# Kernel tuning notes

Hardware: AMD Instinct MI355X
Metric: run time of the kernel (lower is better)

Reference implementation:

```python
import jax, jax.numpy as jnp
import numpy as np

N_BINS = 15  # init kwarg n_bins


def setup_inputs() -> dict:
    key = jax.random.key(0)
    k1, k2, k3, k4 = jax.random.split(key, 4)
    B, T = 8192, 4096
    confidences = jax.random.uniform(k1, (B, T), dtype=jnp.float32)
    predictions = jax.random.randint(k2, (B, T), 0, 3, dtype=jnp.int32)
    targets = jax.random.randint(k3, (B, T), 0, 3, dtype=jnp.int32)
    mask = jax.random.randint(k4, (B, T), 0, 2, dtype=jnp.int32)
    return {"confidences": confidences, "predictions": predictions,
            "targets": targets, "mask": mask}


def reference(confidences, predictions, targets, mask):
    # Flatten, as in the torch forward.
    c = confidences.reshape(-1)
    p = predictions.reshape(-1)
    t = targets.reshape(-1)
    w = mask.reshape(-1).astype(c.dtype)  # 1.0 where valid, 0.0 where masked out

    n = N_BINS
    # Bin b covers (b/n, (b+1)/n]: for c in (0,1], bin index = ceil(c*n) - 1.
    idx = jnp.clip(jnp.ceil(c * n).astype(jnp.int32) - 1, 0, n - 1)
    # c == 0 falls in no bin (strict lower bound on first bin), c > 1 in none.
    in_range = ((c > 0.0) & (c <= 1.0)).astype(c.dtype)
    wv = w * in_range  # effective per-element weight for bin statistics

    counts = jax.ops.segment_sum(wv, idx, num_segments=n)              # n_b
    conf_sum = jax.ops.segment_sum(wv * c, idx, num_segments=n)        # sum conf per bin
    corr = (p == t).astype(c.dtype)
    corr_sum = jax.ops.segment_sum(wv * corr, idx, num_segments=n)     # sum correct per bin

    total = jnp.sum(w)  # len(confidences) after masking
    safe = jnp.maximum(counts, jnp.asarray(1.0, c.dtype))
    avg_conf = conf_sum / safe
    acc = corr_sum / safe
    ece = jnp.sum(jnp.where(counts > 0, jnp.abs(avg_conf - acc) * counts / total, 0.0))
    return ece
```

## Files before the change

kernel.cpp:

```cpp
#include <hip/hip_runtime.h>

#define NBINS 15

typedef float f32x4 __attribute__((ext_vector_type(4)));
typedef int   i32x4 __attribute__((ext_vector_type(4)));


__global__ __launch_bounds__(256, 8) void ece_partial(
    const float* __restrict__ conf,
    const int*   __restrict__ pred,
    const int*   __restrict__ targ,
    const int*   __restrict__ mask,
    unsigned long long* __restrict__ ws,
    int nvec)
{
    __shared__ unsigned int h[4][16];
    __shared__ unsigned long long stot;

    const int tid = threadIdx.x;
    const int wid = tid >> 6;

    if (tid < 64) h[tid >> 4][tid & 15] = 0u;
    if (tid == 0) stot = 0ULL;
    __syncthreads();

    const int gid    = blockIdx.x * blockDim.x + tid;
    const int stride = gridDim.x * blockDim.x;

    const f32x4* __restrict__ c4p = (const f32x4*)conf;
    const i32x4* __restrict__ p4p = (const i32x4*)pred;
    const i32x4* __restrict__ t4p = (const i32x4*)targ;
    const i32x4* __restrict__ m4p = (const i32x4*)mask;

    unsigned int tot = 0;

    int i = gid;
    for (; i + stride < nvec; i += 2 * stride) {
        const int j = i + stride;
        f32x4 c0 = c4p[i];
        f32x4 c1 = c4p[j];
        i32x4 p0 = p4p[i];
        i32x4 p1 = p4p[j];
        i32x4 t0 = t4p[i];
        i32x4 t1 = t4p[j];
        i32x4 m0 = m4p[i];
        i32x4 m1 = m4p[j];
        asm volatile("" : "+v"(c0), "+v"(c1), "+v"(p0), "+v"(p1),
                          "+v"(t0), "+v"(t1), "+v"(m0), "+v"(m1));

#pragma unroll
        for (int k = 0; k < 4; ++k) {
            float c = c0[k];
            int   m = m0[k];
            tot += (unsigned int)m;
            if ((m != 0) & (c > 0.0f) & (c <= 1.0f)) {
                int bin = (int)ceilf(c * 15.0f) - 1;
                bin = min(max(bin, 0), NBINS - 1);
                float corr = (p0[k] == t0[k]) ? 1.0f : 0.0f;
                int d = (int)rintf((c - corr) * 65536.0f);
                atomicAdd(&h[wid][bin], (unsigned int)d);
            }
        }
#pragma unroll
        for (int k = 0; k < 4; ++k) {
            float c = c1[k];
            int   m = m1[k];
            tot += (unsigned int)m;
            if ((m != 0) & (c > 0.0f) & (c <= 1.0f)) {
                int bin = (int)ceilf(c * 15.0f) - 1;
                bin = min(max(bin, 0), NBINS - 1);
                float corr = (p1[k] == t1[k]) ? 1.0f : 0.0f;
                int d = (int)rintf((c - corr) * 65536.0f);
                atomicAdd(&h[wid][bin], (unsigned int)d);
            }
        }
    }
    for (; i < nvec; i += stride) {
        f32x4 c0 = c4p[i];
        i32x4 p0 = p4p[i];
        i32x4 t0 = t4p[i];
        i32x4 m0 = m4p[i];
#pragma unroll
        for (int k = 0; k < 4; ++k) {
            float c = c0[k];
            int   m = m0[k];
            tot += (unsigned int)m;
            if ((m != 0) & (c > 0.0f) & (c <= 1.0f)) {
                int bin = (int)ceilf(c * 15.0f) - 1;
                bin = min(max(bin, 0), NBINS - 1);
                float corr = (p0[k] == t0[k]) ? 1.0f : 0.0f;
                int d = (int)rintf((c - corr) * 65536.0f);
                atomicAdd(&h[wid][bin], (unsigned int)d);
            }
        }
    }

    unsigned int v = tot;
#pragma unroll
    for (int off = 32; off; off >>= 1) v += __shfl_down(v, off, 64);
    if ((tid & 63) == 0) atomicAdd(&stot, (unsigned long long)v);

    __syncthreads();

    if (tid < NBINS) {
        int s = (int)(h[0][tid] + h[1][tid] + h[2][tid] + h[3][tid]);
        if (s != 0)
            atomicAdd(&ws[tid], (unsigned long long)(long long)s);
    }
    if (tid == 0) {
        unsigned long long s = stot;
        if (s) atomicAdd(&ws[NBINS], s);
    }
}

__global__ void ece_scalar_tail(const float* __restrict__ conf,
                                const int*   __restrict__ pred,
                                const int*   __restrict__ targ,
                                const int*   __restrict__ mask,
                                unsigned long long* __restrict__ ws,
                                long long start, long long n)
{
    long long i = start + threadIdx.x;
    if (i < n) {
        float c = conf[i];
        int   m = mask[i];
        if (m) atomicAdd(&ws[NBINS], 1ULL);
        if ((m != 0) & (c > 0.0f) & (c <= 1.0f)) {
            int bin = (int)ceilf(c * 15.0f) - 1;
            bin = min(max(bin, 0), NBINS - 1);
            float corr = (pred[i] == targ[i]) ? 1.0f : 0.0f;
            int d = (int)rintf((c - corr) * 65536.0f);
            atomicAdd(&ws[bin], (unsigned long long)(long long)d);
        }
    }
}

__global__ void ece_final(const unsigned long long* __restrict__ ws,
                          float* __restrict__ out)
{
    int tid = threadIdx.x;
    double v = 0.0;
    if (tid < NBINS) {
        long long s = (long long)ws[tid];
        v = fabs((double)s);
    }
#pragma unroll
    for (int off = 32; off; off >>= 1) v += __shfl_down(v, off, 64);
    if (tid == 0) {
        double total = (double)ws[NBINS];
        if (total < 1.0) total = 1.0;
        out[0] = (float)(v * (1.0 / 65536.0) / total);
    }
}

extern "C" void kernel_launch(void* const* d_in, const int* in_sizes, int n_in,
                              void* d_out, int out_size, void* d_ws, size_t ws_size,
                              hipStream_t stream)
{
    const float* conf = (const float*)d_in[0];
    const int*   pred = (const int*)d_in[1];
    const int*   targ = (const int*)d_in[2];
    const int*   mask = (const int*)d_in[3];
    long long n    = in_sizes[0];
    int       nvec = (int)(n / 4);

    unsigned long long* ws = (unsigned long long*)d_ws;

    hipMemsetAsync(d_ws, 0, (NBINS + 1) * sizeof(unsigned long long), stream);

    ece_partial<<<2048, 256, 0, stream>>>(conf, pred, targ, mask, ws, nvec);
    if (n % 4 != 0) {
        ece_scalar_tail<<<1, 64, 0, stream>>>(conf, pred, targ, mask, ws,
                                              (long long)nvec * 4, n);
    }
    ece_final<<<1, 64, 0, stream>>>(ws, (float*)d_out);
}
```

Measured before the change: 118.2 us.

## Replace shared-memory histogram atomics with per-thread register bin accumulators

Each thread now keeps 15 private integer accumulators and adds each element's fixed-point contribution through a branchless compare-select across all bins. The accumulators are then reduced across each wavefront with shuffles before a few shared atomics. This removes the heavily contended per-element LDS atomics, at the cost of much more VALU work per element and higher register pressure. The launch bounds and grid size are also reduced to match the lower occupancy.

```diff
diff --git a/kernel.cpp b/kernel.cpp
--- a/kernel.cpp
+++ b/kernel.cpp
@@ -6,7 +6,7 @@
 typedef int   i32x4 __attribute__((ext_vector_type(4)));
 
 
-__global__ __launch_bounds__(256, 8) void ece_partial(
+__global__ __launch_bounds__(256, 6) void ece_partial(
     const float* __restrict__ conf,
     const int*   __restrict__ pred,
     const int*   __restrict__ targ,
@@ -14,13 +14,13 @@
     unsigned long long* __restrict__ ws,
     int nvec)
 {
-    __shared__ unsigned int h[4][16];
+    __shared__ unsigned int hsum[16];
     __shared__ unsigned long long stot;
 
-    const int tid = threadIdx.x;
-    const int wid = tid >> 6;
+    const int tid  = threadIdx.x;
+    const int lane = tid & 63;
 
-    if (tid < 64) h[tid >> 4][tid & 15] = 0u;
+    if (tid < 16) hsum[tid] = 0u;
     if (tid == 0) stot = 0ULL;
     __syncthreads();
 
@@ -31,6 +31,10 @@
     const i32x4* __restrict__ p4p = (const i32x4*)pred;
     const i32x4* __restrict__ t4p = (const i32x4*)targ;
     const i32x4* __restrict__ m4p = (const i32x4*)mask;
+
+    int acc[NBINS];
+#pragma unroll
+    for (int b = 0; b < NBINS; ++b) acc[b] = 0;
 
     unsigned int tot = 0;
 
@@ -53,26 +57,30 @@
             float c = c0[k];
             int   m = m0[k];
             tot += (unsigned int)m;
-            if ((m != 0) & (c > 0.0f) & (c <= 1.0f)) {
-                int bin = (int)ceilf(c * 15.0f) - 1;
-                bin = min(max(bin, 0), NBINS - 1);
-                float corr = (p0[k] == t0[k]) ? 1.0f : 0.0f;
-                int d = (int)rintf((c - corr) * 65536.0f);
-                atomicAdd(&h[wid][bin], (unsigned int)d);
-            }
+            bool valid = (m != 0) & (c > 0.0f) & (c <= 1.0f);
+            int bin = (int)ceilf(c * 15.0f) - 1;
+            bin = min(max(bin, 0), NBINS - 1);
+            bin = valid ? bin : -1;
+            float corr = (p0[k] == t0[k]) ? 1.0f : 0.0f;
+            int d = (int)rintf((c - corr) * 65536.0f);
+#pragma unroll
+            for (int b = 0; b < NBINS; ++b)
+                acc[b] += (bin == b) ? d : 0;
         }
 #pragma unroll
         for (int k = 0; k < 4; ++k) {
             float c = c1[k];
             int   m = m1[k];
             tot += (unsigned int)m;
-            if ((m != 0) & (c > 0.0f) & (c <= 1.0f)) {
-                int bin = (int)ceilf(c * 15.0f) - 1;
-                bin = min(max(bin, 0), NBINS - 1);
-                float corr = (p1[k] == t1[k]) ? 1.0f : 0.0f;
-                int d = (int)rintf((c - corr) * 65536.0f);
-                atomicAdd(&h[wid][bin], (unsigned int)d);
-            }
+            bool valid = (m != 0) & (c > 0.0f) & (c <= 1.0f);
+            int bin = (int)ceilf(c * 15.0f) - 1;
+            bin = min(max(bin, 0), NBINS - 1);
+            bin = valid ? bin : -1;
+            float corr = (p1[k] == t1[k]) ? 1.0f : 0.0f;
+            int d = (int)rintf((c - corr) * 65536.0f);
+#pragma unroll
+            for (int b = 0; b < NBINS; ++b)
+                acc[b] += (bin == b) ? d : 0;
         }
     }
     for (; i < nvec; i += stride) {
@@ -85,25 +93,39 @@
             float c = c0[k];
             int   m = m0[k];
             tot += (unsigned int)m;
-            if ((m != 0) & (c > 0.0f) & (c <= 1.0f)) {
-                int bin = (int)ceilf(c * 15.0f) - 1;
-                bin = min(max(bin, 0), NBINS - 1);
-                float corr = (p0[k] == t0[k]) ? 1.0f : 0.0f;
-                int d = (int)rintf((c - corr) * 65536.0f);
-                atomicAdd(&h[wid][bin], (unsigned int)d);
-            }
+            bool valid = (m != 0) & (c > 0.0f) & (c <= 1.0f);
+            int bin = (int)ceilf(c * 15.0f) - 1;
+            bin = min(max(bin, 0), NBINS - 1);
+            bin = valid ? bin : -1;
+            float corr = (p0[k] == t0[k]) ? 1.0f : 0.0f;
+            int d = (int)rintf((c - corr) * 65536.0f);
+#pragma unroll
+            for (int b = 0; b < NBINS; ++b)
+                acc[b] += (bin == b) ? d : 0;
         }
     }
 
+#pragma unroll
+    for (int b = 0; b < NBINS; ++b) {
+        int v = acc[b];
+#pragma unroll
+        for (int off = 32; off; off >>= 1) v += __shfl_down(v, off, 64);
+        acc[b] = v;
+    }
     unsigned int v = tot;
 #pragma unroll
     for (int off = 32; off; off >>= 1) v += __shfl_down(v, off, 64);
-    if ((tid & 63) == 0) atomicAdd(&stot, (unsigned long long)v);
 
+    if (lane == 0) {
+#pragma unroll
+        for (int b = 0; b < NBINS; ++b)
+            if (acc[b] != 0) atomicAdd(&hsum[b], (unsigned int)acc[b]);
+        atomicAdd(&stot, (unsigned long long)v);
+    }
     __syncthreads();
 
     if (tid < NBINS) {
-        int s = (int)(h[0][tid] + h[1][tid] + h[2][tid] + h[3][tid]);
+        int s = (int)hsum[tid];
         if (s != 0)
             atomicAdd(&ws[tid], (unsigned long long)(long long)s);
     }
@@ -168,7 +190,7 @@
 
     hipMemsetAsync(d_ws, 0, (NBINS + 1) * sizeof(unsigned long long), stream);
 
-    ece_partial<<<2048, 256, 0, stream>>>(conf, pred, targ, mask, ws, nvec);
+    ece_partial<<<1536, 256, 0, stream>>>(conf, pred, targ, mask, ws, nvec);
     if (n % 4 != 0) {
         ece_scalar_tail<<<1, 64, 0, stream>>>(conf, pred, targ, mask, ws,
                                               (long long)nvec * 4, n);
```

Result: no change. 116.6 us (-1.4%).
